# Optimization experiments

Measured on AMD Instinct MI355X. Metric: run time of the kernel, lower is better.

The kernel has to match this reference:

```python
import jax, jax.numpy as jnp
import numpy as np

TEMPERATURE = 0.07
NUM_UNIFY_CLASSES = 256


def setup_inputs() -> dict:
    key = jax.random.key(0)
    k1, k2, k3 = jax.random.split(key, 3)
    b, c, h, w = 16, 256, 128, 128
    # small-magnitude feats so exp(logits) stays finite at temperature 0.07
    feats = jax.random.normal(k1, (b, c, h, w), dtype=jnp.float32) * 0.05
    queue = jax.random.normal(k2, (NUM_UNIFY_CLASSES, c), dtype=jnp.float32)
    queue = queue / jnp.linalg.norm(queue, axis=1, keepdims=True)  # unit rows, as a memory bank would hold
    labels = jax.random.randint(k3, (b * h * w, NUM_UNIFY_CLASSES), 0, 2, dtype=jnp.int32)
    return {"feats": feats, "queue": queue, "labels": labels}


def reference(feats, queue, labels):
    b, c, h, w = feats.shape
    # [b,c,h,w] -> [N, c]
    f = jnp.transpose(feats, (0, 2, 3, 1)).reshape(-1, c)
    # [N, M] logits
    logits = (f @ queue.T) / TEMPERATURE
    pos_mask = labels.reshape(-1, NUM_UNIFY_CLASSES).astype(logits.dtype)
    neg_mask = 1.0 - pos_mask
    sum_neg = jnp.sum(jnp.exp(logits) * neg_mask, axis=1)   # [N]
    sum_pos = jnp.sum(jnp.exp(-logits) * pos_mask, axis=1)  # [N]
    loss = jnp.log(sum_neg * sum_pos + 1.0)                 # [N]
    lb_num = jnp.sum(loss != 0)
    return jnp.where(lb_num == 0, jnp.float32(0.0),
                     jnp.sum(loss) / jnp.maximum(lb_num, 1).astype(loss.dtype))
```

## Files before the change

kernel.cpp:

```cpp
#include <hip/hip_runtime.h>
#include <hip/hip_bf16.h>


typedef __bf16 bf16x8 __attribute__((ext_vector_type(8)));
typedef float floatx4 __attribute__((ext_vector_type(4)));

__device__ __forceinline__ unsigned int pack_bf2(float a, float b) {
  unsigned int ua = __float_as_uint(a) + 0x8000u;
  unsigned int ub = __float_as_uint(b) + 0x8000u;
  return (ua >> 16) | (ub & 0xffff0000u);
}

__global__ void qprep(const float* __restrict__ queue,
                      unsigned short* __restrict__ qs,
                      float* __restrict__ accum) {
  const int gt = blockIdx.x * 256 + threadIdx.x;
  const int t = gt >> 6;
  const int lane = gt & 63;
  const int m = ((t >> 3) << 4) | (lane & 15);
  const int k0 = ((t & 7) << 5) | ((lane >> 4) << 3);
  const float* qr = queue + m * 256 + k0;
  const float TINV = 14.2857142857142857f;
  union { unsigned int u32[4]; uint4 v; } u;
#pragma unroll
  for (int j = 0; j < 4; ++j)
    u.u32[j] = pack_bf2(qr[2 * j] * TINV, qr[2 * j + 1] * TINV);
  *(uint4*)(qs + (size_t)gt * 8) = u.v;
  if (gt == 0) { accum[0] = 0.0f; accum[1] = 0.0f; }
}

__global__ __launch_bounds__(256, 4) void pcl_main(
    const float* __restrict__ feats,
    const int* __restrict__ labels,
    const unsigned short* __restrict__ qs,
    float* __restrict__ accum) {
  __shared__ uint4 Bs[2048];
  __shared__ float Red[8][64];

  const int bx = blockIdx.x;
  const int bidx = bx >> 8;
  const int hw0 = (bx & 255) << 6;
  const int tid = threadIdx.x;
  const int w = tid >> 6;
  const int lane = tid & 63;
  const int qd = lane >> 4;
  const int s = lane & 15;

  const float* gbase = feats + (size_t)bidx * 4194304 + (size_t)hw0;
  float f[64];
#pragma unroll
  for (int i = 0; i < 64; ++i)
    f[i] = gbase[(size_t)((w << 6) + i) * 16384 + lane];

#pragma unroll
  for (int g = 0; g < 8; ++g) {
    uint4 u;
    u.x = pack_bf2(f[8 * g + 0], f[8 * g + 1]);
    u.y = pack_bf2(f[8 * g + 2], f[8 * g + 3]);
    u.z = pack_bf2(f[8 * g + 4], f[8 * g + 5]);
    u.w = pack_bf2(f[8 * g + 6], f[8 * g + 7]);
    const int kg = (w << 3) + g;
    Bs[(((kg >> 2) << 2) + qd) * 64 + ((kg & 3) << 4) + s] = u;
  }

  floatx4 acc[4][4];
#pragma unroll
  for (int mt = 0; mt < 4; ++mt)
#pragma unroll
    for (int nt = 0; nt < 4; ++nt)
      acc[mt][nt] = floatx4{0.0f, 0.0f, 0.0f, 0.0f};

  __syncthreads();

  const bf16x8* qfrag = (const bf16x8*)qs;
  const bf16x8* Bf = (const bf16x8*)Bs;
#pragma unroll
  for (int ks = 0; ks < 8; ++ks) {
    bf16x8 af[4];
#pragma unroll
    for (int mt = 0; mt < 4; ++mt)
      af[mt] = qfrag[(((((w << 2) + mt) << 3) | ks) << 6) + lane];
    bf16x8 bfv[4];
#pragma unroll
    for (int nt = 0; nt < 4; ++nt)
      bfv[nt] = Bf[(((ks << 2) + nt) << 6) + lane];
#pragma unroll
    for (int mt = 0; mt < 4; ++mt)
#pragma unroll
      for (int nt = 0; nt < 4; ++nt)
        acc[mt][nt] = __builtin_amdgcn_mfma_f32_16x16x32_bf16(af[mt], bfv[nt],
                                                              acc[mt][nt], 0, 0, 0);
  }

  const size_t nbase = (size_t)bx << 6;
  const int cbase = (w << 6) | (qd << 2);

  float nn[4] = {0.f, 0.f, 0.f, 0.f};
  float pp[4] = {0.f, 0.f, 0.f, 0.f};

  int4 labA[4], labB[4];
#pragma unroll
  for (int nt = 0; nt < 4; ++nt)
    labA[nt] = *(const int4*)(labels + ((nbase + (nt << 4) + s) << 8) + cbase);

#define TERM(LV, AV, NTI)                                   \
  do {                                                      \
    const bool p_ = (LV) != 0;                              \
    const float l_ = (AV);                                  \
    const float e_ = __expf(p_ ? -l_ : l_);                 \
    nn[NTI] += p_ ? 0.0f : e_;                              \
    pp[NTI] += p_ ? e_ : 0.0f;                              \
  } while (0)

#pragma unroll
  for (int mt = 0; mt < 4; ++mt) {
    const int4* cur = (mt & 1) ? labB : labA;
    int4* nxt = (mt & 1) ? labA : labB;
    if (mt < 3) {
#pragma unroll
      for (int nt = 0; nt < 4; ++nt)
        nxt[nt] = *(const int4*)(labels + ((nbase + (nt << 4) + s) << 8) +
                                 cbase + ((mt + 1) << 4));
    }
#pragma unroll
    for (int nt = 0; nt < 4; ++nt) {
      const int4 lb = cur[nt];
      const floatx4 a = acc[mt][nt];
      TERM(lb.x, a[0], nt);
      TERM(lb.y, a[1], nt);
      TERM(lb.z, a[2], nt);
      TERM(lb.w, a[3], nt);
    }
  }
#undef TERM

#pragma unroll
  for (int nt = 0; nt < 4; ++nt) {
    nn[nt] += __shfl_xor(nn[nt], 16);
    nn[nt] += __shfl_xor(nn[nt], 32);
    pp[nt] += __shfl_xor(pp[nt], 16);
    pp[nt] += __shfl_xor(pp[nt], 32);
  }
  if (lane < 16) {
#pragma unroll
    for (int nt = 0; nt < 4; ++nt) {
      Red[(w << 1) | 0][(nt << 4) + lane] = nn[nt];
      Red[(w << 1) | 1][(nt << 4) + lane] = pp[nt];
    }
  }
  __syncthreads();

  if (tid < 64) {
    const float sn = Red[0][tid] + Red[2][tid] + Red[4][tid] + Red[6][tid];
    const float sp = Red[1][tid] + Red[3][tid] + Red[5][tid] + Red[7][tid];
    float loss = logf(sn * sp + 1.0f);
    float c = (loss != 0.0f) ? 1.0f : 0.0f;
#pragma unroll
    for (int off = 32; off > 0; off >>= 1) {
      loss += __shfl_xor(loss, off);
      c += __shfl_xor(c, off);
    }
    if (tid == 0) {
      atomicAdd(&accum[0], loss);
      atomicAdd(&accum[1], c);
    }
  }
}

__global__ void pcl_finalize(const float* __restrict__ accum,
                             float* __restrict__ out) {
  const float ssum = accum[0];
  const float c = accum[1];
  out[0] = (c != 0.0f) ? (ssum / c) : 0.0f;
}

extern "C" void kernel_launch(void* const* d_in, const int* in_sizes, int n_in,
                              void* d_out, int out_size, void* d_ws, size_t ws_size,
                              hipStream_t stream) {
  (void)in_sizes; (void)n_in; (void)out_size; (void)ws_size;
  const float* feats = (const float*)d_in[0];
  const float* queue = (const float*)d_in[1];
  const int* labels = (const int*)d_in[2];

  unsigned short* qs = (unsigned short*)d_ws;
  float* accum = (float*)((char*)d_ws + 256 * 256 * sizeof(unsigned short));

  qprep<<<32, 256, 0, stream>>>(queue, qs, accum);
  pcl_main<<<4096, 256, 0, stream>>>(feats, labels, qs, accum);
  pcl_finalize<<<1, 1, 0, stream>>>(accum, (float*)d_out);
}
```

Measured before the change: 537.8 us.

## Issue all label loads upfront with feats and compress them to bitmasks

All 16 int4 label loads per thread now issue at kernel start, together with the feature loads, so their latency overlaps the bf16 packing and MFMA work instead of following the GEMM. The labels are packed into two 32-bit masks so the 64 label registers die before the accumulators go live. The sign flip for positive entries becomes an XOR on the float bits. To make room for the extra early registers, launch bounds drop from 4 to 3 waves per SIMD, which lowers occupancy.

New measurement: 566.4 us. 1.05x slower.

```diff
diff --git a/kernel.cpp b/kernel.cpp
--- a/kernel.cpp
+++ b/kernel.cpp
@@ -29,7 +29,7 @@
   if (gt == 0) { accum[0] = 0.0f; accum[1] = 0.0f; }
 }
 
-__global__ __launch_bounds__(256, 4) void pcl_main(
+__global__ __launch_bounds__(256, 3) void pcl_main(
     const float* __restrict__ feats,
     const int* __restrict__ labels,
     const unsigned short* __restrict__ qs,
@@ -46,11 +46,21 @@
   const int qd = lane >> 4;
   const int s = lane & 15;
 
-  const float* gbase = feats + (size_t)bidx * 4194304 + (size_t)hw0;
+  const float* gb = feats + (size_t)bidx * 4194304 + (size_t)hw0 + lane;
   float f[64];
 #pragma unroll
   for (int i = 0; i < 64; ++i)
-    f[i] = gbase[(size_t)((w << 6) + i) * 16384 + lane];
+    f[i] = gb[(size_t)((w << 6) + i) * 16384];
+
+  const size_t nbase = (size_t)bx << 6;
+  const int cbase = (w << 6) | (qd << 2);
+  int4 labv[16];
+#pragma unroll
+  for (int mt = 0; mt < 4; ++mt)
+#pragma unroll
+    for (int nt = 0; nt < 4; ++nt)
+      labv[(mt << 2) + nt] =
+          *(const int4*)(labels + ((nbase + (nt << 4) + s) << 8) + cbase + (mt << 4));
 
 #pragma unroll
   for (int g = 0; g < 8; ++g) {
@@ -61,6 +71,19 @@
     u.w = pack_bf2(f[8 * g + 6], f[8 * g + 7]);
     const int kg = (w << 3) + g;
     Bs[(((kg >> 2) << 2) + qd) * 64 + ((kg & 3) << 4) + s] = u;
+  }
+
+  unsigned int m0 = 0, m1 = 0;
+#pragma unroll
+  for (int mt = 0; mt < 4; ++mt) {
+#pragma unroll
+    for (int nt = 0; nt < 4; ++nt) {
+      const int4 lb = labv[(mt << 2) + nt];
+      const unsigned int b = ((mt & 1) << 4) | (nt << 2);
+      unsigned int bits = ((lb.x != 0) ? 1u : 0u) | ((lb.y != 0) ? 2u : 0u) |
+                          ((lb.z != 0) ? 4u : 0u) | ((lb.w != 0) ? 8u : 0u);
+      if (mt < 2) m0 |= bits << b; else m1 |= bits << b;
+    }
   }
 
   floatx4 acc[4][4];
@@ -92,47 +115,25 @@
                                                               acc[mt][nt], 0, 0, 0);
   }
 
-  const size_t nbase = (size_t)bx << 6;
-  const int cbase = (w << 6) | (qd << 2);
-
   float nn[4] = {0.f, 0.f, 0.f, 0.f};
   float pp[4] = {0.f, 0.f, 0.f, 0.f};
-
-  int4 labA[4], labB[4];
-#pragma unroll
-  for (int nt = 0; nt < 4; ++nt)
-    labA[nt] = *(const int4*)(labels + ((nbase + (nt << 4) + s) << 8) + cbase);
-
-#define TERM(LV, AV, NTI)                                   \
-  do {                                                      \
-    const bool p_ = (LV) != 0;                              \
-    const float l_ = (AV);                                  \
-    const float e_ = __expf(p_ ? -l_ : l_);                 \
-    nn[NTI] += p_ ? 0.0f : e_;                              \
-    pp[NTI] += p_ ? e_ : 0.0f;                              \
-  } while (0)
-
 #pragma unroll
   for (int mt = 0; mt < 4; ++mt) {
-    const int4* cur = (mt & 1) ? labB : labA;
-    int4* nxt = (mt & 1) ? labA : labB;
-    if (mt < 3) {
-#pragma unroll
-      for (int nt = 0; nt < 4; ++nt)
-        nxt[nt] = *(const int4*)(labels + ((nbase + (nt << 4) + s) << 8) +
-                                 cbase + ((mt + 1) << 4));
-    }
+    const unsigned int mm = (mt < 2) ? m0 : m1;
 #pragma unroll
     for (int nt = 0; nt < 4; ++nt) {
-      const int4 lb = cur[nt];
       const floatx4 a = acc[mt][nt];
-      TERM(lb.x, a[0], nt);
-      TERM(lb.y, a[1], nt);
-      TERM(lb.z, a[2], nt);
-      TERM(lb.w, a[3], nt);
+      const unsigned int base = ((mt & 1) << 4) | (nt << 2);
+#pragma unroll
+      for (int c = 0; c < 4; ++c) {
+        const unsigned int p = (mm >> (base + c)) & 1u;
+        const float ls = __uint_as_float(__float_as_uint(a[c]) ^ (p << 31));
+        const float e = __expf(ls);
+        nn[nt] += p ? 0.0f : e;
+        pp[nt] += p ? e : 0.0f;
+      }
     }
   }
-#undef TERM
 
 #pragma unroll
   for (int nt = 0; nt < 4; ++nt) {
```
